# Kernel optimization log

Measured on AMD Instinct MI355X. Metric: run time of the kernel, lower is better.

## Reference

```python
import jax, jax.numpy as jnp
import numpy as np

B, N, G, P, L = 2, 6, 4, 8, 4
CIN, COUT = 256, 128
CIMG = COUT // G  # 32 per-group image channels
CAMC = 64
GX, GY, GZ = 64, 64, 4
Q = 8192
RES = (0.6, 0.6, 0.4)
PR = (-19.2, -19.2, -1.0)
IMG_W, IMG_H = 704.0, 256.0
FEAT_HW = [(32, 88), (16, 44), (8, 22), (4, 11)]


def setup_inputs():
    key = jax.random.key(0)
    ks = jax.random.split(key, 20)
    inp = {}
    for l, (H, W) in enumerate(FEAT_HW):
        inp[f"feat{l}"] = jax.random.normal(ks[l], (B, N, G * CIMG, H, W), jnp.float32)
    inp["pts_bev"] = jax.random.normal(ks[4], (B, CIN, GY, GX), jnp.float32)
    inp["lidar2img"] = jax.random.normal(ks[5], (B, N, 4, 4), jnp.float32)
    inp["query_mask"] = jnp.ones((B, Q), jnp.float32)
    inp["vox_x"] = jax.random.randint(ks[6], (B, Q), 0, GX, jnp.int32)
    inp["vox_y"] = jax.random.randint(ks[7], (B, Q), 0, GY, jnp.int32)
    inp["vox_z"] = jax.random.randint(ks[8], (B, Q), 0, GZ, jnp.int32)
    inp["w_offset"] = 0.02 * jax.random.normal(ks[9], (CIN, G * P * 3), jnp.float32)
    inp["b_offset"] = jax.random.uniform(ks[10], (G * P * 3,), jnp.float32, -0.5, 0.5)
    inp["w_scale"] = 0.02 * jax.random.normal(ks[11], (CIN, G * P * L), jnp.float32)
    inp["b_scale"] = jnp.zeros((G * P * L,), jnp.float32)
    inp["w_agg"] = 0.02 * jax.random.normal(ks[12], (P * COUT, COUT), jnp.float32)
    inp["b_agg"] = jnp.zeros((COUT,), jnp.float32)
    inp["conv1_w"] = 0.02 * jax.random.normal(ks[13], (CAMC * GZ, COUT * GZ, 3, 3), jnp.float32)
    inp["conv2_w"] = 0.02 * jax.random.normal(ks[14], (512, CAMC * GZ, 3, 3), jnp.float32)
    inp["conv3_w"] = 0.02 * jax.random.normal(ks[15], (512, 512, 3, 3), jnp.float32)
    inp["conv4_w"] = 0.02 * jax.random.normal(ks[16], (COUT, 512, 3, 3), jnp.float32)
    for i, c in zip(range(1, 5), (CAMC * GZ, 512, 512, COUT)):
        inp[f"bn{i}_g"] = jnp.ones((c,), jnp.float32)
        inp[f"bn{i}_b"] = jnp.zeros((c,), jnp.float32)
    return inp


def _bilinear(feat, bg, view, u, v):
    # feat: [BG, N, H, W, C]; u, v normalized to [0,1]; zero padding, align_corners=False
    H, W = feat.shape[2], feat.shape[3]
    px = u * W - 0.5
    py = v * H - 0.5
    x0f = jnp.floor(px)
    y0f = jnp.floor(py)
    wx = px - x0f
    wy = py - y0f
    x0 = x0f.astype(jnp.int32)
    y0 = y0f.astype(jnp.int32)

    def g(xi, yi):
        ok = ((xi >= 0) & (xi < W) & (yi >= 0) & (yi < H)).astype(feat.dtype)
        val = feat[bg, view, jnp.clip(yi, 0, H - 1), jnp.clip(xi, 0, W - 1)]
        return val * ok[..., None]

    return (g(x0, y0) * ((1 - wx) * (1 - wy))[..., None]
            + g(x0 + 1, y0) * (wx * (1 - wy))[..., None]
            + g(x0, y0 + 1) * ((1 - wx) * wy)[..., None]
            + g(x0 + 1, y0 + 1) * (wx * wy)[..., None])


def _conv_bn_relu(x, w, g, b):
    y = jax.lax.conv_general_dilated(x, w, (1, 1), 'SAME',
                                     dimension_numbers=('NCHW', 'OIHW', 'NCHW'))
    # eval-mode BatchNorm with running_mean=0, running_var=1
    y = y * (g / np.float32(np.sqrt(1.0 + 1e-5)))[None, :, None, None] + b[None, :, None, None]
    return jax.nn.relu(y)


def reference(feat0, feat1, feat2, feat3, pts_bev, lidar2img, query_mask,
              w_offset, b_offset, w_scale, b_scale, w_agg, b_agg,
              conv1_w, bn1_g, bn1_b, conv2_w, bn2_g, bn2_b,
              conv3_w, bn3_g, bn3_b, conv4_w, bn4_g, bn4_b,
              vox_x, vox_y, vox_z):
    GP = G * P
    bidx = jnp.arange(B)[:, None]
    # sparse voxel gather of BEV point features (pts_feat[i, y, x])
    pts_f = pts_bev.transpose(0, 2, 3, 1)[bidx, vox_y, vox_x]  # [B,Q,CIN]
    off = (pts_f @ w_offset + b_offset).reshape(B, Q, GP, 3)
    sw = jax.nn.softmax((pts_f @ w_scale + b_scale).reshape(B, Q, GP, L), axis=-1)
    # frustum voxel-center coords
    coord = jnp.stack([(vox_x + 0.5) * RES[0] + PR[0],
                       (vox_y + 0.5) * RES[1] + PR[1],
                       (vox_z + 0.5) * RES[2] + PR[2]], axis=-1).astype(jnp.float32)
    # make_sample_points: xy scaled by res[0], z by res[2]
    delta = off * jnp.array([RES[0], RES[0], RES[2]], jnp.float32)
    sxyz = coord[:, :, None, :] + delta  # [B,Q,GP,3]
    sp4 = jnp.concatenate([sxyz, jnp.ones_like(sxyz[..., :1])], axis=-1)
    cam = jnp.einsum('bnij,bqpj->bnqpi', lidar2img, sp4)  # [B,N,Q,GP,4]
    homo = jnp.maximum(cam[..., 2:3], 1e-5)
    uv = cam[..., 0:2] / homo / jnp.array([IMG_W, IMG_H], jnp.float32)
    valid = ((cam[..., 2] > 1e-5) & (uv[..., 0] > 0.0) & (uv[..., 0] < 1.0)
             & (uv[..., 1] > 0.0) & (uv[..., 1] < 1.0)).astype(jnp.float32)
    valid = valid.transpose(0, 2, 3, 1)  # [B,Q,GP,N]
    i_view = jnp.argmax(valid, axis=-1)  # [B,Q,GP]
    uv_q = uv.transpose(0, 2, 3, 1, 4)  # [B,Q,GP,N,2]
    idx = jnp.broadcast_to(i_view[..., None, None], (B, Q, GP, 1, 2))
    uv_sel = jnp.take_along_axis(uv_q, idx, axis=3)[..., 0, :]  # [B,Q,GP,2]
    # split heads/groups -> [B*G, Q, P, *]
    uv_bg = uv_sel.reshape(B, Q, G, P, 2).transpose(0, 2, 1, 3, 4).reshape(B * G, Q, P, 2)
    view_bg = i_view.reshape(B, Q, G, P).transpose(0, 2, 1, 3).reshape(B * G, Q, P)
    sw_bg = sw.reshape(B, Q, G, P, L).transpose(0, 2, 1, 3, 4).reshape(B * G, Q, P, L)
    bg = jnp.arange(B * G)[:, None, None]
    # msmv_sampling: multi-level multi-view bilinear sampling + softmax level weights
    out = jnp.zeros((B * G, Q, P, CIMG), jnp.float32)
    for l, f in enumerate((feat0, feat1, feat2, feat3)):
        H, W = f.shape[3], f.shape[4]
        fv = f.reshape(B, N, G, CIMG, H, W).transpose(0, 2, 1, 4, 5, 3).reshape(B * G, N, H, W, CIMG)
        out = out + sw_bg[..., l:l + 1] * _bilinear(fv, bg, view_bg, uv_bg[..., 0], uv_bg[..., 1])
    # [B,G,Q,P,C] -> [B,Q,P,G,C] -> flatten (matches final.permute(0,2,4,1,3).flatten(2))
    final = out.reshape(B, G, Q, P, CIMG).transpose(0, 2, 3, 1, 4).reshape(B, Q, P * G * CIMG)
    agg = final @ w_agg + b_agg  # [B,Q,COUT]
    # scatter back into dense BEV grid
    ffeat = jnp.zeros((B, GZ, GY, GX, COUT), jnp.float32)
    ffeat = ffeat.at[bidx, vox_z, vox_y, vox_x].add(agg * query_mask[..., None])
    x = ffeat.transpose(0, 4, 1, 2, 3).reshape(B, COUT * GZ, GY, GX)
    x = _conv_bn_relu(x, conv1_w, bn1_g, bn1_b)
    x = _conv_bn_relu(x, conv2_w, bn2_g, bn2_b)
    x = _conv_bn_relu(x, conv3_w, bn3_g, bn3_b)
    return _conv_bn_relu(x, conv4_w, bn4_g, bn4_b)
```

## Files before the change

### kernel.cpp

```cpp
#include <hip/hip_runtime.h>
#include <math.h>

#define NB    2
#define NQ    8192
#define NCIN  256
#define NG    4
#define NP    8
#define NGP   32
#define NCIMG 32
#define NCOUT 128
#define NVIEW 6
#define GXD   64
#define GYD   64
#define GZD   4

typedef float f32x4 __attribute__((ext_vector_type(4)));
typedef short s16x8 __attribute__((ext_vector_type(8)));
typedef unsigned short u16;
typedef unsigned int   u32;

__device__ __forceinline__ u16 bf16_rne(float f) {
    u32 u = __float_as_uint(f);
    u32 r = (u + 0x7FFFu + ((u >> 16) & 1u)) >> 16;
    return (u16)r;
}
__device__ __forceinline__ float bf16_f(u16 h) {
    return __uint_as_float(((u32)h) << 16);
}

__global__ void transpose_feat(const float* __restrict__ src, float* __restrict__ dst,
                               int H, int W)
{
    const int total = NB * NG * NVIEW * H * W * 32;
    for (int i = blockIdx.x * blockDim.x + threadIdx.x; i < total;
         i += gridDim.x * blockDim.x) {
        int c = i & 31;
        int r = i >> 5;
        int x = r % W;  r /= W;
        int y = r % H;  r /= H;
        int n = r % NVIEW; r /= NVIEW;
        int g = r & 3;  r >>= 2;
        int b = r;
        dst[i] = src[(((size_t)(b * NVIEW + n) * 128 + g * 32 + c) * H + y) * W + x];
    }
}

__global__ void pack_wT(const float* __restrict__ w_off, const float* __restrict__ w_sc,
                        float* __restrict__ wT)
{
    int i = blockIdx.x * 256 + threadIdx.x;
    if (i >= 224 * 256) return;
    int col = i >> 8, k = i & 255;
    wT[i] = (col < 96) ? w_off[k * 96 + col] : w_sc[k * 128 + (col - 96)];
}

__global__ void pack_conv_w(const float* __restrict__ src, u16* __restrict__ hi,
                            u16* __restrict__ lo, int CI, int CO)
{
    const int N = CO * CI * 9;
    for (int i = blockIdx.x * blockDim.x + threadIdx.x; i < N;
         i += gridDim.x * blockDim.x) {
        int tap = i % 9;
        int r = i / 9;
        int ci = r % CI;
        int co = r / CI;
        float v = src[i];
        u16 h = bf16_rne(v);
        size_t d = ((size_t)tap * CO + co) * CI + ci;
        hi[d] = h;
        lo[d] = bf16_rne(v - bf16_f(h));
    }
}

__device__ __forceinline__ float tapf(const float* __restrict__ base, int H, int W,
                                      int x, int y, int c)
{
    if ((unsigned)x >= (unsigned)W || (unsigned)y >= (unsigned)H) return 0.f;
    return base[(size_t)(y * W + x) * 32 + c];
}

__device__ __forceinline__ float bilin(const float* __restrict__ base, int H, int W,
                                       float u, float v, int c)
{
    float px = u * (float)W - 0.5f;
    float py = v * (float)H - 0.5f;
    px = fminf(fmaxf(px, -1.0e8f), 1.0e8f);
    py = fminf(fmaxf(py, -1.0e8f), 1.0e8f);
    float x0f = floorf(px), y0f = floorf(py);
    float wx = px - x0f, wy = py - y0f;
    int x0 = (int)x0f, y0 = (int)y0f;
    float v00 = tapf(base, H, W, x0,     y0,     c);
    float v10 = tapf(base, H, W, x0 + 1, y0,     c);
    float v01 = tapf(base, H, W, x0,     y0 + 1, c);
    float v11 = tapf(base, H, W, x0 + 1, y0 + 1, c);
    return v00 * (1.f - wx) * (1.f - wy) + v10 * wx * (1.f - wy)
         + v01 * (1.f - wx) * wy         + v11 * wx * wy;
}

__global__ __launch_bounds__(256) void fused_query4(
    const float* __restrict__ pts_bev, const float* __restrict__ l2i,
    const float* __restrict__ qmask,
    const float* __restrict__ wT, const float* __restrict__ b_off,
    const float* __restrict__ b_sc,
    const float* __restrict__ w_agg, const float* __restrict__ b_agg,
    const int* __restrict__ vxp, const int* __restrict__ vyp, const int* __restrict__ vzp,
    const float* __restrict__ fT0, const float* __restrict__ fT1,
    const float* __restrict__ fT2, const float* __restrict__ fT3,
    float* __restrict__ xout_cl)
{
    const int bq = blockIdx.x;
    const int q0 = bq << 2;
    const int b  = q0 >> 13;
    const int t  = threadIdx.x;

    __shared__ float s_pts[4][NCIN];
    __shared__ float s_off[4][96];
    __shared__ float s_sw[4][128];
    __shared__ float s_u[4][NGP], s_v[4][NGP];
    __shared__ int   s_view[4][NGP];
    __shared__ float s_l2i[96];
    __shared__ float s_final[4][1024];
    __shared__ float s_red[4][256];
    __shared__ int   s_vx[4], s_vy[4], s_vz[4];
    __shared__ float s_qm[4];

    if (t < 4) {
        s_vx[t] = vxp[q0 + t]; s_vy[t] = vyp[q0 + t]; s_vz[t] = vzp[q0 + t];
        s_qm[t] = qmask[q0 + t];
    }
    if (t < 96) s_l2i[t] = l2i[b * 96 + t];
    __syncthreads();

    for (int i = t; i < 4 * NCIN; i += 256) {
        int qi = i >> 8, c = i & 255;
        s_pts[qi][c] = pts_bev[((size_t)(b * NCIN + c) * GYD + s_vy[qi]) * GXD + s_vx[qi]];
    }
    __syncthreads();

    if (t < 224) {
        const float* __restrict__ wrow = wT + t * 256;
        float bias = (t < 96) ? b_off[t] : b_sc[t - 96];
        float a0 = bias, a1 = bias, a2 = bias, a3 = bias;
        #pragma unroll 8
        for (int k = 0; k < NCIN; ++k) {
            float wk = wrow[k];
            a0 = fmaf(s_pts[0][k], wk, a0);
            a1 = fmaf(s_pts[1][k], wk, a1);
            a2 = fmaf(s_pts[2][k], wk, a2);
            a3 = fmaf(s_pts[3][k], wk, a3);
        }
        if (t < 96) {
            s_off[0][t] = a0; s_off[1][t] = a1; s_off[2][t] = a2; s_off[3][t] = a3;
        } else {
            int c2 = t - 96;
            s_sw[0][c2] = a0; s_sw[1][c2] = a1; s_sw[2][c2] = a2; s_sw[3][c2] = a3;
        }
    }
    __syncthreads();

    if (t < 128) {
        const int q = t >> 5, gp = t & 31;
        float a0 = s_sw[q][gp * 4 + 0], a1 = s_sw[q][gp * 4 + 1];
        float a2 = s_sw[q][gp * 4 + 2], a3 = s_sw[q][gp * 4 + 3];
        float m  = fmaxf(fmaxf(a0, a1), fmaxf(a2, a3));
        float e0 = expf(a0 - m), e1 = expf(a1 - m), e2 = expf(a2 - m), e3 = expf(a3 - m);
        float inv = 1.f / (e0 + e1 + e2 + e3);
        s_sw[q][gp * 4 + 0] = e0 * inv; s_sw[q][gp * 4 + 1] = e1 * inv;
        s_sw[q][gp * 4 + 2] = e2 * inv; s_sw[q][gp * 4 + 3] = e3 * inv;

        float cx = ((float)s_vx[q] + 0.5f) * 0.6f - 19.2f;
        float cy = ((float)s_vy[q] + 0.5f) * 0.6f - 19.2f;
        float cz = ((float)s_vz[q] + 0.5f) * 0.4f - 1.0f;
        float sx = cx + s_off[q][gp * 3 + 0] * 0.6f;
        float sy = cy + s_off[q][gp * 3 + 1] * 0.6f;
        float sz = cz + s_off[q][gp * 3 + 2] * 0.4f;

        int best = 0; float bu = 0.f, bv = 0.f; bool found = false;
        #pragma unroll
        for (int n = 0; n < NVIEW; ++n) {
            const float* M = &s_l2i[n * 16];
            float px = M[0] * sx + M[1] * sy + M[2]  * sz + M[3];
            float py = M[4] * sx + M[5] * sy + M[6]  * sz + M[7];
            float pz = M[8] * sx + M[9] * sy + M[10] * sz + M[11];
            float homo = fmaxf(pz, 1e-5f);
            float u = px / homo / 704.0f;
            float v = py / homo / 256.0f;
            bool val = (pz > 1e-5f) && (u > 0.f) && (u < 1.f) && (v > 0.f) && (v < 1.f);
            if (n == 0) { bu = u; bv = v; }
            if (val && !found) { found = true; best = n; bu = u; bv = v; }
        }
        s_view[q][gp] = best; s_u[q][gp] = bu; s_v[q][gp] = bv;
    }
    __syncthreads();

    for (int i = t; i < 4096; i += 256) {
        const int q = i >> 10, item = i & 1023;
        const int gp = item >> 5, c = item & 31;
        const int g = gp >> 3, p = gp & 7;
        const int view = s_view[q][gp];
        const float u = s_u[q][gp], v = s_v[q][gp];
        const size_t bgv = (size_t)((b * NG + g) * NVIEW + view);
        float acc = 0.f;
        acc += s_sw[q][gp * 4 + 0] * bilin(fT0 + bgv * (32 * 88 * 32), 32, 88, u, v, c);
        acc += s_sw[q][gp * 4 + 1] * bilin(fT1 + bgv * (16 * 44 * 32), 16, 44, u, v, c);
        acc += s_sw[q][gp * 4 + 2] * bilin(fT2 + bgv * ( 8 * 22 * 32),  8, 22, u, v, c);
        acc += s_sw[q][gp * 4 + 3] * bilin(fT3 + bgv * ( 4 * 11 * 32),  4, 11, u, v, c);
        s_final[q][(p * NG + g) * NCIMG + c] = acc;
    }
    __syncthreads();

    {
        const int co = t & 127, k0 = (t >> 7) * 512;
        float a0 = 0.f, a1 = 0.f, a2 = 0.f, a3 = 0.f;
        #pragma unroll 8
        for (int k = 0; k < 512; ++k) {
            float wv = w_agg[(size_t)(k0 + k) * NCOUT + co];
            a0 = fmaf(s_final[0][k0 + k], wv, a0);
            a1 = fmaf(s_final[1][k0 + k], wv, a1);
            a2 = fmaf(s_final[2][k0 + k], wv, a2);
            a3 = fmaf(s_final[3][k0 + k], wv, a3);
        }
        s_red[0][t] = a0; s_red[1][t] = a1; s_red[2][t] = a2; s_red[3][t] = a3;
    }
    __syncthreads();
    if (t < 128) {
        #pragma unroll
        for (int q = 0; q < 4; ++q) {
            float val = s_red[q][t] + s_red[q][t + 128] + b_agg[t];
            val *= s_qm[q];
            atomicAdd(&xout_cl[((size_t)(b * 4096) + s_vy[q] * 64 + s_vx[q]) * 512
                               + t * 4 + s_vz[q]], val);
        }
    }
}

__global__ __launch_bounds__(256) void conv3x3_mfma(
    const float* __restrict__ xin, const u16* __restrict__ whi,
    const u16* __restrict__ wlo,
    const float* __restrict__ gam, const float* __restrict__ bet,
    float* __restrict__ yout, int CI, int CO)
{
    const int b   = blockIdx.x >> 6;
    const int y0  = blockIdx.x & 63;
    const int cob = blockIdx.y;
    const int t = threadIdx.x;
    const int w = t >> 6, l = t & 63;
    const int l15 = l & 15, kg = l >> 4;

    __shared__ __align__(16) u16 lds_hi[3 * 66 * 32];
    __shared__ __align__(16) u16 lds_lo[3 * 66 * 32];

    const int co_lane = cob * 64 + w * 16 + l15;

    f32x4 acc[4];
    #pragma unroll
    for (int m = 0; m < 4; ++m) acc[m] = (f32x4){0.f, 0.f, 0.f, 0.f};

    for (int cc = 0; cc < CI; cc += 32) {
        __syncthreads();
        for (int i = t; i < 792; i += 256) {
            const int cb = i & 3, r2 = i >> 2;
            const int xl = r2 % 66, r = r2 / 66;
            const int yi = y0 - 1 + r, xi = xl - 1;
            float v[8];
            if ((unsigned)yi < 64u && (unsigned)xi < 64u) {
                const float4* p = reinterpret_cast<const float4*>(
                    xin + ((size_t)(b * 4096 + yi * 64 + xi) * CI + cc + cb * 8));
                float4 f0 = p[0], f1 = p[1];
                v[0] = f0.x; v[1] = f0.y; v[2] = f0.z; v[3] = f0.w;
                v[4] = f1.x; v[5] = f1.y; v[6] = f1.z; v[7] = f1.w;
            } else {
                #pragma unroll
                for (int j = 0; j < 8; ++j) v[j] = 0.f;
            }
            union { u16 u[8]; uint4 q; } H, L;
            #pragma unroll
            for (int j = 0; j < 8; ++j) {
                u16 h = bf16_rne(v[j]);
                H.u[j] = h;
                L.u[j] = bf16_rne(v[j] - bf16_f(h));
            }
            const int off = (r * 66 + xl) * 32 + ((cb ^ ((xl ^ (xl >> 2)) & 3)) << 3);
            *reinterpret_cast<uint4*>(&lds_hi[off]) = H.q;
            *reinterpret_cast<uint4*>(&lds_lo[off]) = L.q;
        }
        __syncthreads();

        #pragma unroll
        for (int tap = 0; tap < 9; ++tap) {
            const int ky = tap / 3, kx = tap % 3;
            const size_t wo = ((size_t)tap * CO + co_lane) * CI + cc + kg * 8;
            const s16x8 Bh = *reinterpret_cast<const s16x8*>(whi + wo);
            const s16x8 Bl = *reinterpret_cast<const s16x8*>(wlo + wo);
            #pragma unroll
            for (int m = 0; m < 4; ++m) {
                const int xl = m * 16 + l15 + kx;
                const int off = (ky * 66 + xl) * 32
                              + ((kg ^ ((xl ^ (xl >> 2)) & 3)) << 3);
                const s16x8 Ah = *reinterpret_cast<const s16x8*>(&lds_hi[off]);
                const s16x8 Al = *reinterpret_cast<const s16x8*>(&lds_lo[off]);
                acc[m] = __builtin_amdgcn_mfma_f32_16x16x32_bf16(Ah, Bh, acc[m], 0, 0, 0);
                acc[m] = __builtin_amdgcn_mfma_f32_16x16x32_bf16(Ah, Bl, acc[m], 0, 0, 0);
                acc[m] = __builtin_amdgcn_mfma_f32_16x16x32_bf16(Al, Bh, acc[m], 0, 0, 0);
            }
        }
    }

    const float gsc = gam[co_lane] * 0.99999500003749978f;
    const float bta = bet[co_lane];
    #pragma unroll
    for (int m = 0; m < 4; ++m) {
        #pragma unroll
        for (int reg = 0; reg < 4; ++reg) {
            const int x = m * 16 + kg * 4 + reg;
            float val = fmaf(acc[m][reg], gsc, bta);
            yout[((size_t)(b * 4096 + y0 * 64 + x)) * CO + co_lane] = fmaxf(val, 0.f);
        }
    }
}

__global__ void to_nchw(const float* __restrict__ xcl, float* __restrict__ out)
{
    const int total = NB * 128 * 4096;
    for (int i = blockIdx.x * blockDim.x + threadIdx.x; i < total;
         i += gridDim.x * blockDim.x) {
        int b = i >> 19;
        int r = i & ((1 << 19) - 1);
        int co = r >> 12;
        int p = r & 4095;
        out[i] = xcl[((size_t)(b << 12) + p) * 128 + co];
    }
}

extern "C" void kernel_launch(void* const* d_in, const int* in_sizes, int n_in,
                              void* d_out, int out_size, void* d_ws, size_t ws_size,
                              hipStream_t stream)
{
    const float* feat0    = (const float*)d_in[0];
    const float* feat1    = (const float*)d_in[1];
    const float* feat2    = (const float*)d_in[2];
    const float* feat3    = (const float*)d_in[3];
    const float* pts_bev  = (const float*)d_in[4];
    const float* l2i      = (const float*)d_in[5];
    const float* qmask    = (const float*)d_in[6];
    const int*   vox_x    = (const int*)d_in[7];
    const int*   vox_y    = (const int*)d_in[8];
    const int*   vox_z    = (const int*)d_in[9];
    const float* w_off    = (const float*)d_in[10];
    const float* b_off    = (const float*)d_in[11];
    const float* w_sc     = (const float*)d_in[12];
    const float* b_sc     = (const float*)d_in[13];
    const float* w_agg    = (const float*)d_in[14];
    const float* b_agg    = (const float*)d_in[15];
    const float* conv1_w  = (const float*)d_in[16];
    const float* conv2_w  = (const float*)d_in[17];
    const float* conv3_w  = (const float*)d_in[18];
    const float* conv4_w  = (const float*)d_in[19];
    const float* bn1_g    = (const float*)d_in[20];
    const float* bn1_b    = (const float*)d_in[21];
    const float* bn2_g    = (const float*)d_in[22];
    const float* bn2_b    = (const float*)d_in[23];
    const float* bn3_g    = (const float*)d_in[24];
    const float* bn3_b    = (const float*)d_in[25];
    const float* bn4_g    = (const float*)d_in[26];
    const float* bn4_b    = (const float*)d_in[27];

    float* ws   = (float*)d_ws;
    float* fT0  = ws;
    float* fT1  = fT0 + 4325376;
    float* fT2  = fT1 + 1081344;
    float* fT3  = fT2 + 270336;
    float* x0cl = ws + 5744640;
    float* x1cl = x0cl + 4194304;
    float* x3cl = x1cl + 2097152;
    float* wT   = x3cl + 4194304;
    float* x2cl = x0cl;
    float* x4cl = x1cl;

    u16* wpk = (u16*)ws;
    u16* wh1 = wpk;            u16* wl1 = wpk + 1179648;
    u16* wh2 = wpk + 2359296;  u16* wl2 = wpk + 3538944;
    u16* wh3 = wpk + 4718592;  u16* wl3 = wpk + 7077888;
    u16* wh4 = wpk + 9437184;  u16* wl4 = wpk + 10027008;

    pack_wT<<<224, 256, 0, stream>>>(w_off, w_sc, wT);

    transpose_feat<<<1024, 256, 0, stream>>>(feat0, fT0, 32, 88);
    transpose_feat<<< 512, 256, 0, stream>>>(feat1, fT1, 16, 44);
    transpose_feat<<< 128, 256, 0, stream>>>(feat2, fT2,  8, 22);
    transpose_feat<<<  64, 256, 0, stream>>>(feat3, fT3,  4, 11);

    hipMemsetAsync(x0cl, 0, (size_t)4194304 * sizeof(float), stream);

    fused_query4<<<NB * NQ / 4, 256, 0, stream>>>(
        pts_bev, l2i, qmask, wT, b_off, b_sc, w_agg, b_agg,
        vox_x, vox_y, vox_z, fT0, fT1, fT2, fT3, x0cl);

    pack_conv_w<<<1024, 256, 0, stream>>>(conv1_w, wh1, wl1, 512, 256);
    pack_conv_w<<<1024, 256, 0, stream>>>(conv2_w, wh2, wl2, 256, 512);
    pack_conv_w<<<2048, 256, 0, stream>>>(conv3_w, wh3, wl3, 512, 512);
    pack_conv_w<<< 512, 256, 0, stream>>>(conv4_w, wh4, wl4, 512, 128);

    conv3x3_mfma<<<dim3(NB * 64, 4), 256, 0, stream>>>(
        x0cl, wh1, wl1, bn1_g, bn1_b, x1cl, 512, 256);
    conv3x3_mfma<<<dim3(NB * 64, 8), 256, 0, stream>>>(
        x1cl, wh2, wl2, bn2_g, bn2_b, x2cl, 256, 512);
    conv3x3_mfma<<<dim3(NB * 64, 8), 256, 0, stream>>>(
        x2cl, wh3, wl3, bn3_g, bn3_b, x3cl, 512, 512);
    conv3x3_mfma<<<dim3(NB * 64, 2), 256, 0, stream>>>(
        x3cl, wh4, wl4, bn4_g, bn4_b, x4cl, 512, 128);

    to_nchw<<<2048, 256, 0, stream>>>(x4cl, (float*)d_out);
}
```

Before: 879.2 us.

## Rewrite query and conv kernels with MFMA aggregation, bf16 split activations, larger tiles

Result: no change. 891.5 us (+1.4%).

```diff
diff --git a/kernel.cpp b/kernel.cpp
--- a/kernel.cpp
+++ b/kernel.cpp
@@ -1,4 +1,5 @@
 #include <hip/hip_runtime.h>
+#include <hip/hip_fp16.h>
 #include <math.h>
 
 #define NB    2
@@ -45,6 +46,25 @@
     }
 }
 
+__global__ __launch_bounds__(256) void transpose_pts(const float* __restrict__ src,
+                                                     float* __restrict__ dst)
+{
+    __shared__ float tile[64][65];
+    const int tid = blockIdx.x;
+    const int b = tid >> 8, rest = tid & 255;
+    const int p0 = (rest >> 2) << 6, c0 = (rest & 3) << 6;
+    const int t = threadIdx.x;
+    for (int i = t; i < 4096; i += 256) {
+        const int c = i >> 6, p = i & 63;
+        tile[c][p] = src[((size_t)(b * 256 + c0 + c) << 12) + p0 + p];
+    }
+    __syncthreads();
+    for (int i = t; i < 4096; i += 256) {
+        const int p = i >> 6, c = i & 63;
+        dst[((size_t)(b * 4096) + p0 + p) * 256 + c0 + c] = tile[c][p];
+    }
+}
+
 __global__ void pack_wT(const float* __restrict__ w_off, const float* __restrict__ w_sc,
                         float* __restrict__ wT)
 {
@@ -52,6 +72,14 @@
     if (i >= 224 * 256) return;
     int col = i >> 8, k = i & 255;
     wT[i] = (col < 96) ? w_off[k * 96 + col] : w_sc[k * 128 + (col - 96)];
+}
+
+__global__ void pack_wagT(const float* __restrict__ w_agg, u16* __restrict__ dst)
+{
+    int i = blockIdx.x * 256 + threadIdx.x;
+    if (i >= 128 * 1024) return;
+    int co = i >> 10, k = i & 1023;
+    dst[i] = bf16_rne(w_agg[k * 128 + co]);
 }
 
 __global__ void pack_conv_w(const float* __restrict__ src, u16* __restrict__ hi,
@@ -72,101 +100,88 @@
     }
 }
 
-__device__ __forceinline__ float tapf(const float* __restrict__ base, int H, int W,
-                                      int x, int y, int c)
-{
-    if ((unsigned)x >= (unsigned)W || (unsigned)y >= (unsigned)H) return 0.f;
-    return base[(size_t)(y * W + x) * 32 + c];
-}
-
-__device__ __forceinline__ float bilin(const float* __restrict__ base, int H, int W,
-                                       float u, float v, int c)
-{
-    float px = u * (float)W - 0.5f;
-    float py = v * (float)H - 0.5f;
-    px = fminf(fmaxf(px, -1.0e8f), 1.0e8f);
-    py = fminf(fmaxf(py, -1.0e8f), 1.0e8f);
-    float x0f = floorf(px), y0f = floorf(py);
-    float wx = px - x0f, wy = py - y0f;
-    int x0 = (int)x0f, y0 = (int)y0f;
-    float v00 = tapf(base, H, W, x0,     y0,     c);
-    float v10 = tapf(base, H, W, x0 + 1, y0,     c);
-    float v01 = tapf(base, H, W, x0,     y0 + 1, c);
-    float v11 = tapf(base, H, W, x0 + 1, y0 + 1, c);
-    return v00 * (1.f - wx) * (1.f - wy) + v10 * wx * (1.f - wy)
-         + v01 * (1.f - wx) * wy         + v11 * wx * wy;
-}
-
-__global__ __launch_bounds__(256) void fused_query4(
-    const float* __restrict__ pts_bev, const float* __restrict__ l2i,
+__global__ void split_x0(const float* __restrict__ x, u16* __restrict__ h,
+                         u16* __restrict__ lo)
+{
+    const int N = NB * 4096 * 512;
+    for (int i = blockIdx.x * blockDim.x + threadIdx.x; i < N;
+         i += gridDim.x * blockDim.x) {
+        float v = x[i];
+        u16 hh = bf16_rne(v);
+        h[i] = hh;
+        lo[i] = bf16_rne(v - bf16_f(hh));
+    }
+}
+
+__global__ __launch_bounds__(256) void fused_query8(
+    const float* __restrict__ pts_cl, const float* __restrict__ l2i,
     const float* __restrict__ qmask,
     const float* __restrict__ wT, const float* __restrict__ b_off,
     const float* __restrict__ b_sc,
-    const float* __restrict__ w_agg, const float* __restrict__ b_agg,
+    const u16* __restrict__ wagT, const float* __restrict__ b_agg,
     const int* __restrict__ vxp, const int* __restrict__ vyp, const int* __restrict__ vzp,
-    const float* __restrict__ fT0, const float* __restrict__ fT1,
-    const float* __restrict__ fT2, const float* __restrict__ fT3,
+    const float* __restrict__ fT,
     float* __restrict__ xout_cl)
 {
-    const int bq = blockIdx.x;
-    const int q0 = bq << 2;
+    const int q0 = blockIdx.x << 3;
     const int b  = q0 >> 13;
     const int t  = threadIdx.x;
 
-    __shared__ float s_pts[4][NCIN];
-    __shared__ float s_off[4][96];
-    __shared__ float s_sw[4][128];
-    __shared__ float s_u[4][NGP], s_v[4][NGP];
-    __shared__ int   s_view[4][NGP];
+    __shared__ float s_pts[8][256];
+    __shared__ float s_off[8][96];
+    __shared__ float s_sw[8][128];
     __shared__ float s_l2i[96];
-    __shared__ float s_final[4][1024];
-    __shared__ float s_red[4][256];
-    __shared__ int   s_vx[4], s_vy[4], s_vz[4];
-    __shared__ float s_qm[4];
-
-    if (t < 4) {
+    __shared__ u32   s_toff[256][16];
+    __shared__ u16   s_twgt[256][16];
+    __shared__ __align__(16) u16 s_fh[8][1024];
+    __shared__ __align__(16) u16 s_fl[8][1024];
+    __shared__ int   s_vx[8], s_vy[8], s_vz[8];
+    __shared__ float s_qm[8];
+
+    if (t < 8) {
         s_vx[t] = vxp[q0 + t]; s_vy[t] = vyp[q0 + t]; s_vz[t] = vzp[q0 + t];
         s_qm[t] = qmask[q0 + t];
     }
     if (t < 96) s_l2i[t] = l2i[b * 96 + t];
     __syncthreads();
 
-    for (int i = t; i < 4 * NCIN; i += 256) {
-        int qi = i >> 8, c = i & 255;
-        s_pts[qi][c] = pts_bev[((size_t)(b * NCIN + c) * GYD + s_vy[qi]) * GXD + s_vx[qi]];
-    }
+    #pragma unroll
+    for (int q = 0; q < 8; ++q)
+        s_pts[q][t] = pts_cl[((size_t)(b * 4096) + s_vy[q] * 64 + s_vx[q]) * 256 + t];
     __syncthreads();
 
     if (t < 224) {
         const float* __restrict__ wrow = wT + t * 256;
-        float bias = (t < 96) ? b_off[t] : b_sc[t - 96];
+        const float bias = (t < 96) ? b_off[t] : b_sc[t - 96];
         float a0 = bias, a1 = bias, a2 = bias, a3 = bias;
-        #pragma unroll 8
-        for (int k = 0; k < NCIN; ++k) {
-            float wk = wrow[k];
-            a0 = fmaf(s_pts[0][k], wk, a0);
-            a1 = fmaf(s_pts[1][k], wk, a1);
-            a2 = fmaf(s_pts[2][k], wk, a2);
-            a3 = fmaf(s_pts[3][k], wk, a3);
+        float a4 = bias, a5 = bias, a6 = bias, a7 = bias;
+        #pragma unroll 4
+        for (int k = 0; k < 256; ++k) {
+            const float wk = wrow[k];
+            a0 = fmaf(s_pts[0][k], wk, a0); a1 = fmaf(s_pts[1][k], wk, a1);
+            a2 = fmaf(s_pts[2][k], wk, a2); a3 = fmaf(s_pts[3][k], wk, a3);
+            a4 = fmaf(s_pts[4][k], wk, a4); a5 = fmaf(s_pts[5][k], wk, a5);
+            a6 = fmaf(s_pts[6][k], wk, a6); a7 = fmaf(s_pts[7][k], wk, a7);
         }
         if (t < 96) {
             s_off[0][t] = a0; s_off[1][t] = a1; s_off[2][t] = a2; s_off[3][t] = a3;
+            s_off[4][t] = a4; s_off[5][t] = a5; s_off[6][t] = a6; s_off[7][t] = a7;
         } else {
-            int c2 = t - 96;
-            s_sw[0][c2] = a0; s_sw[1][c2] = a1; s_sw[2][c2] = a2; s_sw[3][c2] = a3;
-        }
-    }
-    __syncthreads();
-
-    if (t < 128) {
+            const int c = t - 96;
+            s_sw[0][c] = a0; s_sw[1][c] = a1; s_sw[2][c] = a2; s_sw[3][c] = a3;
+            s_sw[4][c] = a4; s_sw[5][c] = a5; s_sw[6][c] = a6; s_sw[7][c] = a7;
+        }
+    }
+    __syncthreads();
+
+    {
         const int q = t >> 5, gp = t & 31;
         float a0 = s_sw[q][gp * 4 + 0], a1 = s_sw[q][gp * 4 + 1];
         float a2 = s_sw[q][gp * 4 + 2], a3 = s_sw[q][gp * 4 + 3];
         float m  = fmaxf(fmaxf(a0, a1), fmaxf(a2, a3));
         float e0 = expf(a0 - m), e1 = expf(a1 - m), e2 = expf(a2 - m), e3 = expf(a3 - m);
         float inv = 1.f / (e0 + e1 + e2 + e3);
-        s_sw[q][gp * 4 + 0] = e0 * inv; s_sw[q][gp * 4 + 1] = e1 * inv;
-        s_sw[q][gp * 4 + 2] = e2 * inv; s_sw[q][gp * 4 + 3] = e3 * inv;
+        const float sw0 = e0 * inv, sw1 = e1 * inv, sw2 = e2 * inv, sw3 = e3 * inv;
 
         float cx = ((float)s_vx[q] + 0.5f) * 0.6f - 19.2f;
         float cy = ((float)s_vy[q] + 0.5f) * 0.6f - 19.2f;
@@ -189,146 +204,196 @@
             if (n == 0) { bu = u; bv = v; }
             if (val && !found) { found = true; best = n; bu = u; bv = v; }
         }
-        s_view[q][gp] = best; s_u[q][gp] = bu; s_v[q][gp] = bv;
-    }
-    __syncthreads();
-
-    for (int i = t; i < 4096; i += 256) {
-        const int q = i >> 10, item = i & 1023;
-        const int gp = item >> 5, c = item & 31;
+
+        const int g = gp >> 3;
+        const u32 bgv = (u32)((b * 4 + g) * 6 + best);
+        auto tapgen = [&](int lidx, int W, int H, u32 lbase, float swl) {
+            float px = fminf(fmaxf(bu * (float)W - 0.5f, -1.0e8f), 1.0e8f);
+            float py = fminf(fmaxf(bv * (float)H - 0.5f, -1.0e8f), 1.0e8f);
+            float x0f = floorf(px), y0f = floorf(py);
+            float wx = px - x0f, wy = py - y0f;
+            int x0 = (int)x0f, y0 = (int)y0f;
+            const u32 base = lbase + bgv * (u32)(H * W * 32);
+            #pragma unroll
+            for (int ti = 0; ti < 4; ++ti) {
+                int xi = x0 + (ti & 1), yi = y0 + (ti >> 1);
+                float bw = ((ti & 1) ? wx : 1.f - wx) * ((ti >> 1) ? wy : 1.f - wy);
+                bool ok = ((unsigned)xi < (unsigned)W) && ((unsigned)yi < (unsigned)H);
+                u32 off = ok ? (base + ((u32)(yi * W + xi) << 5)) : 0u;
+                float wgt = ok ? swl * bw : 0.f;
+                s_toff[t][lidx * 4 + ti] = off;
+                s_twgt[t][lidx * 4 + ti] = __half_as_ushort(__float2half(wgt));
+            }
+        };
+        tapgen(0, 88, 32, 0u,       sw0);
+        tapgen(1, 44, 16, 4325376u, sw1);
+        tapgen(2, 22,  8, 5406720u, sw2);
+        tapgen(3, 11,  4, 5677056u, sw3);
+    }
+    __syncthreads();
+
+    for (int i = t; i < 8192; i += 256) {
+        const int pair = i >> 5, c = i & 31;
+        float acc = 0.f;
+        #pragma unroll
+        for (int tp = 0; tp < 16; ++tp) {
+            const u32 off = s_toff[pair][tp];
+            const float wgt = __half2float(__ushort_as_half(s_twgt[pair][tp]));
+            acc = fmaf(wgt, fT[off + c], acc);
+        }
+        const int gp = pair & 31, q = pair >> 5;
         const int g = gp >> 3, p = gp & 7;
-        const int view = s_view[q][gp];
-        const float u = s_u[q][gp], v = s_v[q][gp];
-        const size_t bgv = (size_t)((b * NG + g) * NVIEW + view);
-        float acc = 0.f;
-        acc += s_sw[q][gp * 4 + 0] * bilin(fT0 + bgv * (32 * 88 * 32), 32, 88, u, v, c);
-        acc += s_sw[q][gp * 4 + 1] * bilin(fT1 + bgv * (16 * 44 * 32), 16, 44, u, v, c);
-        acc += s_sw[q][gp * 4 + 2] * bilin(fT2 + bgv * ( 8 * 22 * 32),  8, 22, u, v, c);
-        acc += s_sw[q][gp * 4 + 3] * bilin(fT3 + bgv * ( 4 * 11 * 32),  4, 11, u, v, c);
-        s_final[q][(p * NG + g) * NCIMG + c] = acc;
+        const int k = ((p << 2) + g) * 32 + c;
+        const u16 h  = bf16_rne(acc);
+        const u16 lo = bf16_rne(acc - bf16_f(h));
+        const int kk = (((k >> 3) ^ q) << 3) | (k & 7);
+        s_fh[q][kk] = h;
+        s_fl[q][kk] = lo;
     }
     __syncthreads();
 
     {
-        const int co = t & 127, k0 = (t >> 7) * 512;
-        float a0 = 0.f, a1 = 0.f, a2 = 0.f, a3 = 0.f;
-        #pragma unroll 8
-        for (int k = 0; k < 512; ++k) {
-            float wv = w_agg[(size_t)(k0 + k) * NCOUT + co];
-            a0 = fmaf(s_final[0][k0 + k], wv, a0);
-            a1 = fmaf(s_final[1][k0 + k], wv, a1);
-            a2 = fmaf(s_final[2][k0 + k], wv, a2);
-            a3 = fmaf(s_final[3][k0 + k], wv, a3);
-        }
-        s_red[0][t] = a0; s_red[1][t] = a1; s_red[2][t] = a2; s_red[3][t] = a3;
-    }
-    __syncthreads();
-    if (t < 128) {
-        #pragma unroll
-        for (int q = 0; q < 4; ++q) {
-            float val = s_red[q][t] + s_red[q][t + 128] + b_agg[t];
-            val *= s_qm[q];
-            atomicAdd(&xout_cl[((size_t)(b * 4096) + s_vy[q] * 64 + s_vx[q]) * 512
-                               + t * 4 + s_vz[q]], val);
-        }
-    }
-}
-
-__global__ __launch_bounds__(256) void conv3x3_mfma(
-    const float* __restrict__ xin, const u16* __restrict__ whi,
-    const u16* __restrict__ wlo,
+        const int wv = t >> 6, l = t & 63;
+        const int l15 = l & 15, kg = l >> 4;
+        f32x4 acc0 = {0.f, 0.f, 0.f, 0.f}, acc1 = {0.f, 0.f, 0.f, 0.f};
+        const u16* __restrict__ B0 = wagT + (((wv * 2) * 16 + l15) << 10);
+        const u16* __restrict__ B1 = wagT + (((wv * 2 + 1) * 16 + l15) << 10);
+        const bool realA = (l15 < 8);
+        for (int ks = 0; ks < 32; ++ks) {
+            s16x8 Ah = {0, 0, 0, 0, 0, 0, 0, 0};
+            s16x8 Al = {0, 0, 0, 0, 0, 0, 0, 0};
+            if (realA) {
+                const int kk = ((((ks << 2) + kg) ^ l15) << 3);
+                Ah = *reinterpret_cast<const s16x8*>(&s_fh[l15][kk]);
+                Al = *reinterpret_cast<const s16x8*>(&s_fl[l15][kk]);
+            }
+            const int ko = (ks << 5) + (kg << 3);
+            const s16x8 Bh0 = *reinterpret_cast<const s16x8*>(B0 + ko);
+            const s16x8 Bh1 = *reinterpret_cast<const s16x8*>(B1 + ko);
+            acc0 = __builtin_amdgcn_mfma_f32_16x16x32_bf16(Ah, Bh0, acc0, 0, 0, 0);
+            acc0 = __builtin_amdgcn_mfma_f32_16x16x32_bf16(Al, Bh0, acc0, 0, 0, 0);
+            acc1 = __builtin_amdgcn_mfma_f32_16x16x32_bf16(Ah, Bh1, acc1, 0, 0, 0);
+            acc1 = __builtin_amdgcn_mfma_f32_16x16x32_bf16(Al, Bh1, acc1, 0, 0, 0);
+        }
+        if (l < 32) {
+            #pragma unroll
+            for (int reg = 0; reg < 4; ++reg) {
+                const int q = kg * 4 + reg;
+                const size_t pbase =
+                    ((size_t)(b * 4096) + s_vy[q] * 64 + s_vx[q]) * 512 + s_vz[q];
+                const float qm = s_qm[q];
+                {
+                    const int co = (wv * 2) * 16 + l15;
+                    atomicAdd(&xout_cl[pbase + co * 4], (acc0[reg] + b_agg[co]) * qm);
+                }
+                {
+                    const int co = (wv * 2 + 1) * 16 + l15;
+                    atomicAdd(&xout_cl[pbase + co * 4], (acc1[reg] + b_agg[co]) * qm);
+                }
+            }
+        }
+    }
+}
+
+template<int ROWS, int NSUB, bool LAST>
+__global__ __launch_bounds__(64 * ROWS * NSUB) void conv3x3_mfma2(
+    const u16* __restrict__ xinh, const u16* __restrict__ xinl,
+    const u16* __restrict__ whi, const u16* __restrict__ wlo,
     const float* __restrict__ gam, const float* __restrict__ bet,
-    float* __restrict__ yout, int CI, int CO)
-{
-    const int b   = blockIdx.x >> 6;
-    const int y0  = blockIdx.x & 63;
-    const int cob = blockIdx.y;
+    u16* __restrict__ youth, u16* __restrict__ youtl,
+    float* __restrict__ ynchw, int CI, int CO)
+{
+    constexpr int STRIPS = 64 / ROWS;
+    constexpr int NTHR = 64 * ROWS * NSUB;
+    constexpr int SR = ROWS + 2;
+    const int b = blockIdx.x / STRIPS, s = blockIdx.x % STRIPS;
+    const int y0 = s * ROWS;
+    const int co0 = blockIdx.y * (NSUB * 32);
     const int t = threadIdx.x;
-    const int w = t >> 6, l = t & 63;
+    const int wid = t >> 6, l = t & 63;
     const int l15 = l & 15, kg = l >> 4;
-
-    __shared__ __align__(16) u16 lds_hi[3 * 66 * 32];
-    __shared__ __align__(16) u16 lds_lo[3 * 66 * 32];
-
-    const int co_lane = cob * 64 + w * 16 + l15;
-
-    f32x4 acc[4];
+    const int r = wid / NSUB, ns = wid % NSUB;
+
+    __shared__ __align__(16) u16 sh[SR * 66 * 32];
+    __shared__ __align__(16) u16 sl[SR * 66 * 32];
+
+    const int coA = co0 + ns * 32 + l15;
+    const int coB = coA + 16;
+
+    f32x4 acc[4][2];
     #pragma unroll
-    for (int m = 0; m < 4; ++m) acc[m] = (f32x4){0.f, 0.f, 0.f, 0.f};
+    for (int m = 0; m < 4; ++m) {
+        acc[m][0] = (f32x4){0.f, 0.f, 0.f, 0.f};
+        acc[m][1] = (f32x4){0.f, 0.f, 0.f, 0.f};
+    }
 
     for (int cc = 0; cc < CI; cc += 32) {
         __syncthreads();
-        for (int i = t; i < 792; i += 256) {
+        for (int i = t; i < SR * 66 * 4; i += NTHR) {
             const int cb = i & 3, r2 = i >> 2;
-            const int xl = r2 % 66, r = r2 / 66;
-            const int yi = y0 - 1 + r, xi = xl - 1;
-            float v[8];
+            const int xx = r2 % 66, rr = r2 / 66;
+            const int yi = y0 - 1 + rr, xi = xx - 1;
+            uint4 H = {0, 0, 0, 0}, L = {0, 0, 0, 0};
             if ((unsigned)yi < 64u && (unsigned)xi < 64u) {
-                const float4* p = reinterpret_cast<const float4*>(
-                    xin + ((size_t)(b * 4096 + yi * 64 + xi) * CI + cc + cb * 8));
-                float4 f0 = p[0], f1 = p[1];
-                v[0] = f0.x; v[1] = f0.y; v[2] = f0.z; v[3] = f0.w;
-                v[4] = f1.x; v[5] = f1.y; v[6] = f1.z; v[7] = f1.w;
-            } else {
-                #pragma unroll
-                for (int j = 0; j < 8; ++j) v[j] = 0.f;
-            }
-            union { u16 u[8]; uint4 q; } H, L;
-            #pragma unroll
-            for (int j = 0; j < 8; ++j) {
-                u16 h = bf16_rne(v[j]);
-                H.u[j] = h;
-                L.u[j] = bf16_rne(v[j] - bf16_f(h));
-            }
-            const int off = (r * 66 + xl) * 32 + ((cb ^ ((xl ^ (xl >> 2)) & 3)) << 3);
-            *reinterpret_cast<uint4*>(&lds_hi[off]) = H.q;
-            *reinterpret_cast<uint4*>(&lds_lo[off]) = L.q;
+                const size_t src = ((size_t)(b * 4096 + yi * 64 + xi)) * CI + cc + cb * 8;
+                H = *reinterpret_cast<const uint4*>(xinh + src);
+                L = *reinterpret_cast<const uint4*>(xinl + src);
+            }
+            const int off = (rr * 66 + xx) * 32 + ((cb ^ ((xx ^ (xx >> 2)) & 3)) << 3);
+            *reinterpret_cast<uint4*>(&sh[off]) = H;
+            *reinterpret_cast<uint4*>(&sl[off]) = L;
         }
         __syncthreads();
 
         #pragma unroll
         for (int tap = 0; tap < 9; ++tap) {
             const int ky = tap / 3, kx = tap % 3;
-            const size_t wo = ((size_t)tap * CO + co_lane) * CI + cc + kg * 8;
-            const s16x8 Bh = *reinterpret_cast<const s16x8*>(whi + wo);
-            const s16x8 Bl = *reinterpret_cast<const s16x8*>(wlo + wo);
+            const size_t woA = ((size_t)tap * CO + coA) * CI + cc + kg * 8;
+            const size_t woB = ((size_t)tap * CO + coB) * CI + cc + kg * 8;
+            const s16x8 BhA = *reinterpret_cast<const s16x8*>(whi + woA);
+            const s16x8 BlA = *reinterpret_cast<const s16x8*>(wlo + woA);
+            const s16x8 BhB = *reinterpret_cast<const s16x8*>(whi + woB);
+            const s16x8 BlB = *reinterpret_cast<const s16x8*>(wlo + woB);
             #pragma unroll
             for (int m = 0; m < 4; ++m) {
-                const int xl = m * 16 + l15 + kx;
-                const int off = (ky * 66 + xl) * 32
-                              + ((kg ^ ((xl ^ (xl >> 2)) & 3)) << 3);
-                const s16x8 Ah = *reinterpret_cast<const s16x8*>(&lds_hi[off]);
-                const s16x8 Al = *reinterpret_cast<const s16x8*>(&lds_lo[off]);
-                acc[m] = __builtin_amdgcn_mfma_f32_16x16x32_bf16(Ah, Bh, acc[m], 0, 0, 0);
-                acc[m] = __builtin_amdgcn_mfma_f32_16x16x32_bf16(Ah, Bl, acc[m], 0, 0, 0);
-                acc[m] = __builtin_amdgcn_mfma_f32_16x16x32_bf16(Al, Bh, acc[m], 0, 0, 0);
-            }
-        }
-    }
-
-    const float gsc = gam[co_lane] * 0.99999500003749978f;
-    const float bta = bet[co_lane];
+                const int xx = m * 16 + l15 + kx;
+                const int off = ((r + ky) * 66 + xx) * 32
+                              + ((kg ^ ((xx ^ (xx >> 2)) & 3)) << 3);
+                const s16x8 Ah = *reinterpret_cast<const s16x8*>(&sh[off]);
+                const s16x8 Al = *reinterpret_cast<const s16x8*>(&sl[off]);
+                acc[m][0] = __builtin_amdgcn_mfma_f32_16x16x32_bf16(Ah, BhA, acc[m][0], 0, 0, 0);
+                acc[m][0] = __builtin_amdgcn_mfma_f32_16x16x32_bf16(Ah, BlA, acc[m][0], 0, 0, 0);
+                acc[m][0] = __builtin_amdgcn_mfma_f32_16x16x32_bf16(Al, BhA, acc[m][0], 0, 0, 0);
+                acc[m][1] = __builtin_amdgcn_mfma_f32_16x16x32_bf16(Ah, BhB, acc[m][1], 0, 0, 0);
+                acc[m][1] = __builtin_amdgcn_mfma_f32_16x16x32_bf16(Ah, BlB, acc[m][1], 0, 0, 0);
+                acc[m][1] = __builtin_amdgcn_mfma_f32_16x16x32_bf16(Al, BhB, acc[m][1], 0, 0, 0);
+            }
+        }
+    }
+
+    const float inv = 0.99999500003749978f;
+    const int row = y0 + r;
     #pragma unroll
-    for (int m = 0; m < 4; ++m) {
+    for (int j = 0; j < 2; ++j) {
+        const int co = j ? coB : coA;
+        const float gsc = gam[co] * inv;
+        const float bta = bet[co];
         #pragma unroll
-        for (int reg = 0; reg < 4; ++reg) {
-            const int x = m * 16 + kg * 4 + reg;
-            float val = fmaf(acc[m][reg], gsc, bta);
-            yout[((size_t)(b * 4096 + y0 * 64 + x)) * CO + co_lane] = fmaxf(val, 0.f);
-        }
-    }
-}
-
-__global__ void to_nchw(const float* __restrict__ xcl, float* __restrict__ out)
-{
-    const int total = NB * 128 * 4096;
-    for (int i = blockIdx.x * blockDim.x + threadIdx.x; i < total;
-         i += gridDim.x * blockDim.x) {
-        int b = i >> 19;
-        int r = i & ((1 << 19) - 1);
-        int co = r >> 12;
-        int p = r & 4095;
-        out[i] = xcl[((size_t)(b << 12) + p) * 128 + co];
+        for (int m = 0; m < 4; ++m) {
+            #pragma unroll
+            for (int reg = 0; reg < 4; ++reg) {
+                const int x = m * 16 + kg * 4 + reg;
+                const float val = fmaxf(fmaf(acc[m][j][reg], gsc, bta), 0.f);
+                if (LAST) {
+                    ynchw[(((size_t)(b * CO + co)) << 12) + row * 64 + x] = val;
+                } else {
+                    const size_t idx = ((size_t)(b * 4096 + row * 64 + x)) * CO + co;
+                    const u16 h = bf16_rne(val);
+                    youth[idx] = h;
+                    youtl[idx] = bf16_rne(val - bf16_f(h));
+                }
+            }
+        }
     }
 }
 
@@ -365,50 +430,54 @@
     const float* bn4_g    = (const float*)d_in[26];
     const float* bn4_b    = (const float*)d_in[27];
 
-    float* ws   = (float*)d_ws;
-    float* fT0  = ws;
-    float* fT1  = fT0 + 4325376;
-    float* fT2  = fT1 + 1081344;
-    float* fT3  = fT2 + 270336;
-    float* x0cl = ws + 5744640;
-    float* x1cl = x0cl + 4194304;
-    float* x3cl = x1cl + 2097152;
-    float* wT   = x3cl + 4194304;
-    float* x2cl = x0cl;
-    float* x4cl = x1cl;
-
-    u16* wpk = (u16*)ws;
-    u16* wh1 = wpk;            u16* wl1 = wpk + 1179648;
-    u16* wh2 = wpk + 2359296;  u16* wl2 = wpk + 3538944;
-    u16* wh3 = wpk + 4718592;  u16* wl3 = wpk + 7077888;
-    u16* wh4 = wpk + 9437184;  u16* wl4 = wpk + 10027008;
-
-    pack_wT<<<224, 256, 0, stream>>>(w_off, w_sc, wT);
+    char* wsb = (char*)d_ws;
+    float* fT0 = (float*)wsb;
+    float* fT1 = fT0 + 4325376;
+    float* fT2 = fT1 + 1081344;
+    float* fT3 = fT2 + 270336;
+    u16* wpk = (u16*)wsb;
+    u16* wh1 = wpk;             u16* wl1 = wpk + 1179648;
+    u16* wh2 = wpk + 2359296;   u16* wl2 = wpk + 3538944;
+    u16* wh3 = wpk + 4718592;   u16* wl3 = wpk + 7077888;
+    u16* wh4 = wpk + 9437184;   u16* wl4 = wpk + 10027008;
+    float* x0f   = (float*)(wsb + 22978560);
+    u16*   x2h   = (u16*)(wsb + 22978560);   u16* x2l = x2h + 4194304;
+    float* ptsCL = (float*)(wsb + 39755776);
+    u16*   x0h   = (u16*)(wsb + 39755776);
+    u16*   x0l   = (u16*)(wsb + 48144384);
+    u16*   x3h   = x0h;                      u16* x3l = x0l;
+    u16*   x1h   = (u16*)(wsb + 56532992);   u16* x1l = x1h + 2097152;
+    u16*   wagT  = (u16*)(wsb + 48144384);
+    float* wTp   = (float*)(wsb + 48406528);
+
+    pack_wT<<<224, 256, 0, stream>>>(w_off, w_sc, wTp);
+    pack_wagT<<<512, 256, 0, stream>>>(w_agg, wagT);
+    transpose_pts<<<512, 256, 0, stream>>>(pts_bev, ptsCL);
 
     transpose_feat<<<1024, 256, 0, stream>>>(feat0, fT0, 32, 88);
     transpose_feat<<< 512, 256, 0, stream>>>(feat1, fT1, 16, 44);
     transpose_feat<<< 128, 256, 0, stream>>>(feat2, fT2,  8, 22);
     transpose_feat<<<  64, 256, 0, stream>>>(feat3, fT3,  4, 11);
 
-    hipMemsetAsync(x0cl, 0, (size_t)4194304 * sizeof(float), stream);
-
-    fused_query4<<<NB * NQ / 4, 256, 0, stream>>>(
-        pts_bev, l2i, qmask, wT, b_off, b_sc, w_agg, b_agg,
-        vox_x, vox_y, vox_z, fT0, fT1, fT2, fT3, x0cl);
+    hipMemsetAsync(x0f, 0, (size_t)4194304 * sizeof(float), stream);
+
+    fused_query8<<<NB * NQ / 8, 256, 0, stream>>>(
+        ptsCL, l2i, qmask, wTp, b_off, b_sc, wagT, b_agg,
+        vox_x, vox_y, vox_z, fT0, x0f);
 
     pack_conv_w<<<1024, 256, 0, stream>>>(conv1_w, wh1, wl1, 512, 256);
     pack_conv_w<<<1024, 256, 0, stream>>>(conv2_w, wh2, wl2, 256, 512);
     pack_conv_w<<<2048, 256, 0, stream>>>(conv3_w, wh3, wl3, 512, 512);
     pack_conv_w<<< 512, 256, 0, stream>>>(conv4_w, wh4, wl4, 512, 128);
 
-    conv3x3_mfma<<<dim3(NB * 64, 4), 256, 0, stream>>>(
-        x0cl, wh1, wl1, bn1_g, bn1_b, x1cl, 512, 256);
-    conv3x3_mfma<<<dim3(NB * 64, 8), 256, 0, stream>>>(
-        x1cl, wh2, wl2, bn2_g, bn2_b, x2cl, 256, 512);
-    conv3x3_mfma<<<dim3(NB * 64, 8), 256, 0, stream>>>(
-        x2cl, wh3, wl3, bn3_g, bn3_b, x3cl, 512, 512);
-    conv3x3_mfma<<<dim3(NB * 64, 2), 256, 0, stream>>>(
-        x3cl, wh4, wl4, bn4_g, bn4_b, x4cl, 512, 128);
-
-    to_nchw<<<2048, 256, 0, stream>>>(x4cl, (float*)d_out);
-}
+    split_x0<<<4096, 256, 0, stream>>>(x0f, x0h, x0l);
+
+    conv3x3_mfma2<2, 2, false><<<dim3(64, 4), 256, 0, stream>>>(
+        x0h, x0l, wh1, wl1, bn1_g, bn1_b, x1h, x1l, nullptr, 512, 256);
+    conv3x3_mfma2<2, 2, false><<<dim3(64, 8), 256, 0, stream>>>(
+        x1h, x1l, wh2, wl2, bn2_g, bn2_b, x2h, x2l, nullptr, 256, 512);
+    conv3x3_mfma2<2, 2, false><<<dim3(64, 8), 256, 0, stream>>>(
+        x2h, x2l, wh3, wl3, bn3_g, bn3_b, x3h, x3l, nullptr, 512, 512);
+    conv3x3_mfma2<1, 2, true><<<dim3(128, 2), 128, 0, stream>>>(
+        x3h, x3l, wh4, wl4, bn4_g, bn4_b, nullptr, nullptr, (float*)d_out, 512, 128);
+}
```
